# Kernel tuning notes

Measured on AMD Instinct MI355X. Metric: run time of the kernel, lower is better.

## Reference

```python
import jax, jax.numpy as jnp
import numpy as np

B = 32768          # batch rows
IN_DIM = 512
HID = 64           # hidden_dim fixed in module
COMM = 128         # output_dim == proto_latent_dim (num_simultaneous_tokens=1)
P = 2048           # num_protos
BETA = 0.25        # settings.alpha != 0
KL_W = 1.0         # settings.kl_weight
ENT_W = 0.1        # settings.entropy_weight
EPSILON = 1e-8


def setup_inputs() -> dict:
    key = jax.random.key(0)
    ks = jax.random.split(key, 16)
    s = 0.05
    return {
        "x": jax.random.normal(ks[0], (B, IN_DIM), jnp.float32),
        "eps": jax.random.normal(ks[1], (B, COMM), jnp.float32),
        "W_emb": jax.random.normal(ks[2], (IN_DIM, HID), jnp.float32) * s,
        "b_emb": jnp.zeros((HID,), jnp.float32),
        "W1": jax.random.normal(ks[3], (HID, HID), jnp.float32) * s,
        "b1": jnp.zeros((HID,), jnp.float32),
        "W2": jax.random.normal(ks[4], (HID, COMM), jnp.float32) * s,
        "b2": jnp.zeros((COMM,), jnp.float32),
        "W_mu": jax.random.normal(ks[5], (COMM, COMM), jnp.float32) * s,
        "b_mu": jnp.zeros((COMM,), jnp.float32),
        "W_var": jax.random.normal(ks[6], (COMM, COMM), jnp.float32) * s,
        "b_var": jnp.zeros((COMM,), jnp.float32),
        "protos": jax.random.uniform(ks[7], (P, COMM), jnp.float32, -1.0 / P, 1.0 / P),
    }


def _sq_dists(a, b):
    # ||a||^2 + ||b||^2 - 2 a b^T  -> [N, P] without [N,P,D] intermediate
    return (jnp.sum(a * a, axis=1, keepdims=True)
            + jnp.sum(b * b, axis=1)
            - 2.0 * a @ b.T)


def reference(x, eps, W_emb, b_emb, W1, b1, W2, b2, W_mu, b_mu, W_var, b_var, protos):
    sg = jax.lax.stop_gradient
    h = x @ W_emb + b_emb                       # [B, HID]
    h = h.reshape(-1, HID)                      # num_imgs = 1
    h = jax.nn.relu(h @ W1 + b1)
    h = jax.nn.relu(h @ W2 + b2)                # [B, COMM]
    r = h.reshape(-1, COMM)
    mu = r @ W_mu + b_mu
    logvar = r @ W_var + b_var
    sample = mu + jnp.exp(0.5 * logvar) * eps   # reparameterize

    # VQ: pairwise squared dists, argmin routing, codebook gather
    dists = _sq_dists(sample, protos)           # [B, P]
    idx = jnp.argmin(dists, axis=1)             # [B]
    quantized = protos[idx]                     # [B, COMM]

    commitment_loss = jnp.mean((sg(quantized) - mu) ** 2)
    embedding_loss = jnp.mean((quantized - sg(mu)) ** 2)
    vq_loss = BETA * commitment_loss + embedding_loss

    # entropy term: softmax-like row probs from Gaussian kernel on mu-proto dists
    # sum(((mu-p)/2)^2, -1) == ||mu-p||^2 / 4, computed via matmul form
    neg_dist = -0.5 * (_sq_dists(mu, protos) / 4.0)
    exponents = jnp.exp(neg_dist) + EPSILON     # [B, P]
    row_probs = exponents / jnp.sum(exponents, axis=1, keepdims=True)
    approx_probs = jnp.mean(row_probs, axis=0)  # [P]
    ent = jnp.sum(-approx_probs * jnp.log(approx_probs))
    vq_loss = vq_loss + ENT_W * ent

    # straight-through estimator
    q_st = sample + sg(quantized - sample)
    output = q_st.reshape(-1, COMM)

    kld = jnp.mean(-0.5 * jnp.sum(1.0 + logvar - mu ** 2 - jnp.exp(logvar), axis=1))
    total_loss = KL_W * kld + vq_loss
    return output, total_loss, kld
```

## Files before the change

### kernel.cpp

```cpp
#include <hip/hip_runtime.h>
#include <cmath>

constexpr int NB   = 32768;
constexpr int IND  = 512;
constexpr int HIDD = 64;
constexpr int CM   = 128;
constexpr int NP   = 2048;
constexpr float BETA  = 0.25f;
constexpr float ENT_W = 0.1f;
constexpr float EPSV  = 1e-8f;

typedef __attribute__((ext_vector_type(8))) short short8v;
typedef __attribute__((ext_vector_type(4))) float f32x4v;

__device__ __forceinline__ float4 ld4(const float* p){ return *reinterpret_cast<const float4*>(p); }
__device__ __forceinline__ void  st4(float* p, float4 v){ *reinterpret_cast<float4*>(p) = v; }

__device__ __forceinline__ unsigned short f2bf(float f){
  union { float f; unsigned u; } v; v.f = f;
  unsigned r = v.u + 0x7fffu + ((v.u >> 16) & 1u);
  return (unsigned short)(r >> 16);
}
__device__ __forceinline__ float bf2f(unsigned short u){
  union { unsigned u; float f; } v; v.u = ((unsigned)u) << 16;
  return v.f;
}
__device__ __forceinline__ short8v cvt8(float4 a, float4 b){
  short8v r;
  r[0]=(short)f2bf(a.x); r[1]=(short)f2bf(a.y); r[2]=(short)f2bf(a.z); r[3]=(short)f2bf(a.w);
  r[4]=(short)f2bf(b.x); r[5]=(short)f2bf(b.y); r[6]=(short)f2bf(b.z); r[7]=(short)f2bf(b.w);
  return r;
}

__device__ __forceinline__ float wave_sum(float v){
  #pragma unroll
  for (int m = 1; m < 64; m <<= 1) v += __shfl_xor(v, m, 64);
  return v;
}

typedef __attribute__((address_space(1))) unsigned int gu32;
typedef __attribute__((address_space(3))) unsigned int su32;
__device__ __forceinline__ void gload_lds16(const void* g, void* s){
  __builtin_amdgcn_global_load_lds((const gu32*)g, (su32*)s, 16, 0, 0);
}
__device__ __forceinline__ void gload_lds4(const void* g, void* s){
  __builtin_amdgcn_global_load_lds((const gu32*)g, (su32*)s, 4, 0, 0);
}
__device__ __forceinline__ void barrier_raw(){
  __builtin_amdgcn_sched_barrier(0);
  __builtin_amdgcn_s_barrier();
  __builtin_amdgcn_sched_barrier(0);
}

__global__ __launch_bounds__(256) void k_prep(const float* __restrict__ protos,
                                              float* __restrict__ normp2,
                                              unsigned short* __restrict__ pBF,
                                              const float* __restrict__ W_emb,
                                              const float* __restrict__ W1,
                                              const float* __restrict__ W2,
                                              const float* __restrict__ Wmu,
                                              const float* __restrict__ Wvar,
                                              unsigned short* __restrict__ WembT,
                                              unsigned short* __restrict__ W1T,
                                              unsigned short* __restrict__ W2T,
                                              unsigned short* __restrict__ WmuT,
                                              unsigned short* __restrict__ WvarT){
  const int b = blockIdx.x, tid = threadIdx.x;
  if (b < 8){
    const int p = b * 256 + tid;
    const float* row = protos + (size_t)p * CM;
    float s = 0.f;
    #pragma unroll
    for (int k = 0; k < CM; k += 4){
      float4 v = ld4(row + k);
      s += v.x*v.x + v.y*v.y + v.z*v.z + v.w*v.w;
      ushort4 u; u.x = f2bf(v.x); u.y = f2bf(v.y); u.z = f2bf(v.z); u.w = f2bf(v.w);
      *reinterpret_cast<ushort4*>(&pBF[(size_t)p * CM + k]) = u;
    }
    normp2[p] = s;
  } else if (b == 8){
    for (int i = tid; i < 512*64; i += 256){
      int k = i >> 6, n = i & 63;
      WembT[n*512 + k] = f2bf(W_emb[i]);
    }
  } else if (b == 9){
    for (int i = tid; i < 64*64; i += 256){
      int k = i >> 6, n = i & 63;
      W1T[n*64 + k] = f2bf(W1[i]);
    }
    for (int i = tid; i < 64*128; i += 256){
      int k = i >> 7, n = i & 127;
      W2T[n*64 + k] = f2bf(W2[i]);
    }
  } else if (b == 10){
    for (int i = tid; i < 128*128; i += 256){
      int k = i >> 7, n = i & 127;
      WmuT[n*128 + k] = f2bf(Wmu[i]);
    }
  } else {
    for (int i = tid; i < 128*128; i += 256){
      int k = i >> 7, n = i & 127;
      WvarT[n*128 + k] = f2bf(Wvar[i]);
    }
  }
}

__global__ __launch_bounds__(256, 2) void fwd_fused(const float* __restrict__ x,
    const unsigned short* __restrict__ WembT, const float* __restrict__ b_emb,
    const unsigned short* __restrict__ W1T,   const float* __restrict__ b1,
    const unsigned short* __restrict__ W2T,   const float* __restrict__ b2,
    const unsigned short* __restrict__ WmuT,  const float* __restrict__ bmu,
    const unsigned short* __restrict__ WvarT, const float* __restrict__ bvar,
    const float* __restrict__ epsIn,
    unsigned short* __restrict__ muBF, unsigned short* __restrict__ sBF,
    float* __restrict__ normMu2, float* __restrict__ kld_part){
  __shared__ __align__(16) unsigned short SH[16384];
  unsigned short* h1s = SH;
  unsigned short* h2s = SH + 4096;
  unsigned short* h3s = SH + 8192;
  unsigned short* muS = SH;
  unsigned short* sS  = SH + 8192;
  __shared__ float redbuf[4];

  const int tid = threadIdx.x;
  const int w = tid >> 6, l = tid & 63;
  const int lr = l >> 4, lc = l & 15;
  const int rowbase = blockIdx.x * 64;
  const int row = w*16 + lc;

  f32x4v acc1[4];
  #pragma unroll
  for (int nt = 0; nt < 4; nt++) acc1[nt] = (f32x4v){0.f,0.f,0.f,0.f};
  #pragma unroll 4
  for (int kc = 0; kc < IND; kc += 32){
    const float* xp = &x[(size_t)(rowbase + row) * IND + kc + lr*8];
    short8v af = cvt8(ld4(xp), ld4(xp + 4));
    #pragma unroll
    for (int nt = 0; nt < 4; nt++){
      const int n = nt*16 + lc;
      short8v bf = *reinterpret_cast<const short8v*>(&WembT[(size_t)n*512 + kc + lr*8]);
      acc1[nt] = __builtin_amdgcn_mfma_f32_16x16x32_bf16(af, bf, acc1[nt], 0, 0, 0);
    }
  }
  #pragma unroll
  for (int nt = 0; nt < 4; nt++){
    const int col = nt*16 + lc;
    const float bb = b_emb[col];
    #pragma unroll
    for (int r = 0; r < 4; r++){
      const int row2 = w*16 + lr*4 + r;
      h1s[(row2*64 + col) ^ ((row2 & 7) << 3)] = f2bf(acc1[nt][r] + bb);
    }
  }
  __syncthreads();

  f32x4v acc2[4];
  #pragma unroll
  for (int nt = 0; nt < 4; nt++) acc2[nt] = (f32x4v){0.f,0.f,0.f,0.f};
  #pragma unroll
  for (int ks = 0; ks < 2; ks++){
    const int ai = (row*64 + ks*32 + lr*8) ^ ((row & 7) << 3);
    short8v af = *reinterpret_cast<const short8v*>(&h1s[ai]);
    #pragma unroll
    for (int nt = 0; nt < 4; nt++){
      const int n = nt*16 + lc;
      short8v bf = *reinterpret_cast<const short8v*>(&W1T[(size_t)n*64 + ks*32 + lr*8]);
      acc2[nt] = __builtin_amdgcn_mfma_f32_16x16x32_bf16(af, bf, acc2[nt], 0, 0, 0);
    }
  }
  __syncthreads();
  #pragma unroll
  for (int nt = 0; nt < 4; nt++){
    const int col = nt*16 + lc;
    const float bb = b1[col];
    #pragma unroll
    for (int r = 0; r < 4; r++){
      const int row2 = w*16 + lr*4 + r;
      h2s[(row2*64 + col) ^ ((row2 & 7) << 3)] = f2bf(fmaxf(acc2[nt][r] + bb, 0.f));
    }
  }
  __syncthreads();

  f32x4v acc3[8];
  #pragma unroll
  for (int nt = 0; nt < 8; nt++) acc3[nt] = (f32x4v){0.f,0.f,0.f,0.f};
  #pragma unroll
  for (int ks = 0; ks < 2; ks++){
    const int ai = (row*64 + ks*32 + lr*8) ^ ((row & 7) << 3);
    short8v af = *reinterpret_cast<const short8v*>(&h2s[ai]);
    #pragma unroll
    for (int nt = 0; nt < 8; nt++){
      const int n = nt*16 + lc;
      short8v bf = *reinterpret_cast<const short8v*>(&W2T[(size_t)n*64 + ks*32 + lr*8]);
      acc3[nt] = __builtin_amdgcn_mfma_f32_16x16x32_bf16(af, bf, acc3[nt], 0, 0, 0);
    }
  }
  #pragma unroll
  for (int nt = 0; nt < 8; nt++){
    const int col = nt*16 + lc;
    const float bb = b2[col];
    #pragma unroll
    for (int r = 0; r < 4; r++){
      const int row2 = w*16 + lr*4 + r;
      h3s[(row2*128 + col) ^ ((row2 & 7) << 3)] = f2bf(fmaxf(acc3[nt][r] + bb, 0.f));
    }
  }
  __syncthreads();

  f32x4v accM[8], accV[8];
  #pragma unroll
  for (int nt = 0; nt < 8; nt++){ accM[nt] = (f32x4v){0.f,0.f,0.f,0.f}; accV[nt] = (f32x4v){0.f,0.f,0.f,0.f}; }
  #pragma unroll
  for (int ks = 0; ks < 4; ks++){
    const int ai = (row*128 + ks*32 + lr*8) ^ ((row & 7) << 3);
    short8v af = *reinterpret_cast<const short8v*>(&h3s[ai]);
    #pragma unroll
    for (int nt = 0; nt < 8; nt++){
      const int n = nt*16 + lc;
      short8v bM = *reinterpret_cast<const short8v*>(&WmuT [(size_t)n*128 + ks*32 + lr*8]);
      short8v bV = *reinterpret_cast<const short8v*>(&WvarT[(size_t)n*128 + ks*32 + lr*8]);
      accM[nt] = __builtin_amdgcn_mfma_f32_16x16x32_bf16(af, bM, accM[nt], 0, 0, 0);
      accV[nt] = __builtin_amdgcn_mfma_f32_16x16x32_bf16(af, bV, accV[nt], 0, 0, 0);
    }
  }
  __syncthreads();

  float kl = 0.f;
  float m2[4] = {0.f, 0.f, 0.f, 0.f};
  #pragma unroll
  for (int nt = 0; nt < 8; nt++){
    const int col = nt*16 + lc;
    const float bm = bmu[col], bv = bvar[col];
    #pragma unroll
    for (int r = 0; r < 4; r++){
      const int row2 = w*16 + lr*4 + r;
      const float mu = accM[nt][r] + bm;
      const float lv = accV[nt][r] + bv;
      const float s2 = __expf(0.5f * lv);
      const float sa = mu + s2 * epsIn[(size_t)(rowbase + row2)*CM + col];
      kl += 1.f + lv - mu*mu - s2*s2;
      m2[r] += mu*mu;
      const int li = (row2*128 + col) ^ ((row2 & 7) << 3);
      muS[li] = f2bf(mu);
      sS [li] = f2bf(sa);
    }
  }
  #pragma unroll
  for (int m = 1; m < 16; m <<= 1){
    #pragma unroll
    for (int r = 0; r < 4; r++) m2[r] += __shfl_xor(m2[r], m, 64);
  }
  if (lc == 0){
    #pragma unroll
    for (int r = 0; r < 4; r++) normMu2[rowbase + w*16 + lr*4 + r] = m2[r];
  }
  const float kw = wave_sum(kl);
  if (l == 0) redbuf[w] = kw;
  __syncthreads();
  if (tid == 0) kld_part[blockIdx.x] = redbuf[0]+redbuf[1]+redbuf[2]+redbuf[3];
  {
    const int r2 = tid >> 2, kq = tid & 3;
    #pragma unroll
    for (int i = 0; i < 4; i++){
      const int k = kq*32 + i*8;
      const int li = (r2*128 + k) ^ ((r2 & 7) << 3);
      short8v vm = *reinterpret_cast<const short8v*>(&muS[li]);
      short8v vs = *reinterpret_cast<const short8v*>(&sS[li]);
      *reinterpret_cast<short8v*>(&muBF[(size_t)(rowbase + r2)*CM + k]) = vm;
      *reinterpret_cast<short8v*>(&sBF [(size_t)(rowbase + r2)*CM + k]) = vs;
    }
  }
}

__global__ __launch_bounds__(512, 4) void proto_merged(
    const unsigned short* __restrict__ sBF, const unsigned short* __restrict__ mBF,
    const unsigned short* __restrict__ pBF, const float* __restrict__ normp2,
    const float* __restrict__ normMu2, const float* __restrict__ protosF,
    float* __restrict__ outA, float* __restrict__ approx_part,
    float* __restrict__ commit_part)
{
  __shared__ __align__(16) unsigned short Ps[3][64*CM];
  __shared__ float Pn[3][64];
  __shared__ float approxl[NP];
  __shared__ float bw[2][64];
  __shared__ int   iw[2][64];
  __shared__ float sw[2][64];
  __shared__ float srow_s[64];
  __shared__ int   bidx_s[64];
  __shared__ float redbuf[8];

  const int tid = threadIdx.x;
  const int w = tid >> 6, l = tid & 63;
  const int lr = l >> 4, lc = l & 15;
  const int rw = w & 1;
  const int pw = (w >> 1) & 1;
  const int mat = w >> 2;
  const int rowbase = blockIdx.x * 64;

  for (int t = tid; t < NP; t += 512) approxl[t] = 0.f;

  const unsigned short* Abase = mat ? mBF : sBF;
  short8v af[2][4];
  #pragma unroll
  for (int mt = 0; mt < 2; mt++){
    const size_t rg = (size_t)(rowbase + rw*32 + mt*16 + lc) * CM;
    #pragma unroll
    for (int ks = 0; ks < 4; ks++)
      af[mt][ks] = *reinterpret_cast<const short8v*>(&Abase[rg + ks*32 + lr*8]);
  }
  float nmn[8];
  #pragma unroll
  for (int mt = 0; mt < 2; mt++)
    #pragma unroll
    for (int r = 0; r < 4; r++)
      nmn[mt*4+r] = -0.125f * normMu2[rowbase + rw*32 + mt*16 + lr*4 + r];

  #define STAGE(pc, buf) {                                                        \
    _Pragma("unroll")                                                             \
    for (int j = 0; j < 2; j++){                                                  \
      const int p = w*8 + j*4 + (l >> 4);                                         \
      const int g = l & 15;                                                       \
      gload_lds16(&pBF[(size_t)((pc) + p)*CM + ((g*8) ^ ((p & 7)*8))],            \
                  &Ps[buf][(w*8 + j*4)*CM]);                                      \
    }                                                                             \
    if (w == 0) gload_lds4(&normp2[(pc) + l], &Pn[buf][0]);                       \
  }
  #define VWAIT_PEND() { if (w == 0) asm volatile("s_waitcnt vmcnt(3)" ::: "memory"); \
                         else        asm volatile("s_waitcnt vmcnt(2)" ::: "memory"); }
  #define VWAIT_ALL()  asm volatile("s_waitcnt vmcnt(0)" ::: "memory")

  float best[8]; int bidx[8]; float sr[8];
  #pragma unroll
  for (int i = 0; i < 8; i++){ best[i] = 3.4e38f; bidx[i] = 0; sr[i] = 0.f; }

  STAGE(0, 0);
  int cur = 0;
  for (int c = 0; c < 32; c++){
    const int nxt = (cur == 2) ? 0 : cur + 1;
    if (c < 31){ STAGE((c+1)*64, nxt); VWAIT_PEND(); }
    else       { VWAIT_ALL(); }
    barrier_raw();
    const float npv0 = Pn[cur][pw*32 + lc];
    const float npv1 = Pn[cur][pw*32 + 16 + lc];
    f32x4v acc[2][2];
    #pragma unroll
    for (int mt = 0; mt < 2; mt++)
      #pragma unroll
      for (int nt = 0; nt < 2; nt++) acc[mt][nt] = (f32x4v){0.f,0.f,0.f,0.f};
    #pragma unroll
    for (int ks = 0; ks < 4; ks++){
      const int pl0 = pw*32 + lc;
      const int pl1 = pw*32 + 16 + lc;
      short8v pf0 = *reinterpret_cast<const short8v*>(&Ps[cur][(pl0*CM + ks*32 + lr*8) ^ ((pl0 & 7) << 3)]);
      short8v pf1 = *reinterpret_cast<const short8v*>(&Ps[cur][(pl1*CM + ks*32 + lr*8) ^ ((pl1 & 7) << 3)]);
      #pragma unroll
      for (int mt = 0; mt < 2; mt++){
        acc[mt][0] = __builtin_amdgcn_mfma_f32_16x16x32_bf16(af[mt][ks], pf0, acc[mt][0], 0, 0, 0);
        acc[mt][1] = __builtin_amdgcn_mfma_f32_16x16x32_bf16(af[mt][ks], pf1, acc[mt][1], 0, 0, 0);
      }
    }
    const int pc = c*64;
    if (mat == 0){
      #pragma unroll
      for (int nt = 0; nt < 2; nt++){
        const int pg = pc + pw*32 + nt*16 + lc;
        const float npv = nt ? npv1 : npv0;
        #pragma unroll
        for (int mt = 0; mt < 2; mt++)
          #pragma unroll
          for (int r = 0; r < 4; r++){
            const float sc = fmaf(-2.f, acc[mt][nt][r], npv);
            if (sc < best[mt*4+r]){ best[mt*4+r] = sc; bidx[mt*4+r] = pg; }
          }
      }
    } else {
      #pragma unroll
      for (int nt = 0; nt < 2; nt++){
        const float pvn = -0.125f * (nt ? npv1 : npv0);
        #pragma unroll
        for (int mt = 0; mt < 2; mt++)
          #pragma unroll
          for (int r = 0; r < 4; r++)
            sr[mt*4+r] += __expf(fmaf(0.25f, acc[mt][nt][r], nmn[mt*4+r] + pvn));
      }
    }
    cur = nxt;
  }

  if (mat == 0){
    #pragma unroll
    for (int m = 1; m < 16; m <<= 1){
      #pragma unroll
      for (int i = 0; i < 8; i++){
        const float ob = __shfl_xor(best[i], m, 64);
        const int   oi = __shfl_xor(bidx[i], m, 64);
        if (ob < best[i] || (ob == best[i] && oi < bidx[i])){ best[i] = ob; bidx[i] = oi; }
      }
    }
    if (lc == 0){
      #pragma unroll
      for (int mt = 0; mt < 2; mt++)
        #pragma unroll
        for (int r = 0; r < 4; r++){
          const int row = rw*32 + mt*16 + lr*4 + r;
          bw[pw][row] = best[mt*4+r];
          iw[pw][row] = bidx[mt*4+r];
        }
    }
  } else {
    #pragma unroll
    for (int m = 1; m < 16; m <<= 1){
      #pragma unroll
      for (int i = 0; i < 8; i++) sr[i] += __shfl_xor(sr[i], m, 64);
    }
    if (lc == 0){
      #pragma unroll
      for (int mt = 0; mt < 2; mt++)
        #pragma unroll
        for (int r = 0; r < 4; r++){
          const int row = rw*32 + mt*16 + lr*4 + r;
          sw[pw][row] = sr[mt*4+r];
        }
    }
  }
  __syncthreads();
  if (tid < 64){
    float b0 = bw[0][tid]; int i0 = iw[0][tid];
    const float b1 = bw[1][tid]; const int i1 = iw[1][tid];
    if (b1 < b0 || (b1 == b0 && i1 < i0)){ b0 = b1; i0 = i1; }
    bidx_s[tid] = i0;
    srow_s[tid] = sw[0][tid] + sw[1][tid] + (float)NP * EPSV;
  }
  STAGE(0, 0);
  __syncthreads();

  {
    const int row = tid >> 3, cp = tid & 7;
    const int rowg = rowbase + row;
    const int idx = bidx_s[row];
    float cl = 0.f;
    #pragma unroll
    for (int c4 = 0; c4 < 4; c4++){
      const int cc = c4*32 + cp*4;
      float4 q = ld4(protosF + (size_t)idx * CM + cc);
      ushort4 mb = *reinterpret_cast<const ushort4*>(&mBF[(size_t)rowg * CM + cc]);
      st4(outA + (size_t)rowg * CM + cc, q);
      const float dx=q.x-bf2f(mb.x), dy=q.y-bf2f(mb.y), dz=q.z-bf2f(mb.z), dw=q.w-bf2f(mb.w);
      cl += dx*dx + dy*dy + dz*dz + dw*dw;
    }
    const float cw = wave_sum(cl);
    if (l == 0) redbuf[w] = cw;
  }
  float rs[8]; float epsc = 0.f;
  #pragma unroll
  for (int mt = 0; mt < 2; mt++)
    #pragma unroll
    for (int r = 0; r < 4; r++){
      rs[mt*4+r] = 1.0f / srow_s[rw*32 + mt*16 + lr*4 + r];
      epsc += rs[mt*4+r];
    }
  epsc *= EPSV;
  if (mat == 0){
    #pragma unroll
    for (int mt = 0; mt < 2; mt++){
      const size_t rg = (size_t)(rowbase + rw*32 + mt*16 + lc) * CM;
      #pragma unroll
      for (int ks = 0; ks < 4; ks++)
        af[mt][ks] = *reinterpret_cast<const short8v*>(&mBF[rg + ks*32 + lr*8]);
    }
  }
  __syncthreads();
  if (tid == 0) commit_part[blockIdx.x] = redbuf[0]+redbuf[1]+redbuf[2]+redbuf[3]
                                        + redbuf[4]+redbuf[5]+redbuf[6]+redbuf[7];

  const int pq = w >> 1;
  cur = 0;
  for (int c = 0; c < 32; c++){
    const int nxt = (cur == 2) ? 0 : cur + 1;
    if (c < 31){ STAGE((c+1)*64, nxt); VWAIT_PEND(); }
    else       { VWAIT_ALL(); }
    barrier_raw();
    const int pl = pq*16 + lc;
    const float npv = Pn[cur][pl];
    f32x4v accB[2];
    accB[0] = (f32x4v){0.f,0.f,0.f,0.f};
    accB[1] = (f32x4v){0.f,0.f,0.f,0.f};
    #pragma unroll
    for (int ks = 0; ks < 4; ks++){
      short8v pf = *reinterpret_cast<const short8v*>(&Ps[cur][(pl*CM + ks*32 + lr*8) ^ ((pl & 7) << 3)]);
      accB[0] = __builtin_amdgcn_mfma_f32_16x16x32_bf16(af[0][ks], pf, accB[0], 0, 0, 0);
      accB[1] = __builtin_amdgcn_mfma_f32_16x16x32_bf16(af[1][ks], pf, accB[1], 0, 0, 0);
    }
    const float pvn = -0.125f * npv;
    float cs = epsc;
    #pragma unroll
    for (int mt = 0; mt < 2; mt++)
      #pragma unroll
      for (int r = 0; r < 4; r++){
        const float e = __expf(fmaf(0.25f, accB[mt][r], nmn[mt*4+r] + pvn));
        cs = fmaf(e, rs[mt*4+r], cs);
      }
    cs += __shfl_xor(cs, 16, 64);
    cs += __shfl_xor(cs, 32, 64);
    if (l < 16) atomicAdd(&approxl[c*64 + pq*16 + lc], cs);
    cur = nxt;
  }
  __syncthreads();
  for (int t = tid; t < NP; t += 512)
    approx_part[(size_t)blockIdx.x * NP + t] = approxl[t];
  #undef STAGE
  #undef VWAIT_PEND
  #undef VWAIT_ALL
}

__global__ __launch_bounds__(256) void k4a(const float* __restrict__ approx_part,
                                           float* __restrict__ ent_part){
  __shared__ float red[128];
  const int tid = threadIdx.x;
  const int p = blockIdx.x * 32 + (tid & 31);
  const int slice = tid >> 5;
  float s = 0.f;
  for (int b = slice; b < 512; b += 8) s += approx_part[(size_t)b * NP + p];
  s += __shfl_xor(s, 32, 64);
  if ((tid & 63) < 32) red[(tid >> 6)*32 + (tid & 31)] = s;
  __syncthreads();
  if (tid < 32){
    const float a = (red[tid] + red[32+tid] + red[64+tid] + red[96+tid]) * (1.0f / 32768.0f);
    float t = -a * logf(a);
    #pragma unroll
    for (int m = 1; m < 32; m <<= 1) t += __shfl_xor(t, m, 32);
    if (tid == 0) ent_part[blockIdx.x] = t;
  }
}

__global__ __launch_bounds__(256) void k4b(const float* __restrict__ kld_part,
                                           const float* __restrict__ commit_part,
                                           const float* __restrict__ ent_part,
                                           float* __restrict__ outs){
  __shared__ float redbuf[8];
  const int tid = threadIdx.x;
  float k = 0.f, c = 0.f;
  for (int i = tid; i < 512; i += 256){ k += kld_part[i]; c += commit_part[i]; }
  float kw = wave_sum(k), cw = wave_sum(c);
  if ((tid & 63) == 0){ redbuf[tid >> 6] = kw; redbuf[4 + (tid >> 6)] = cw; }
  __syncthreads();
  if (tid == 0){
    float ks = redbuf[0] + redbuf[1] + redbuf[2] + redbuf[3];
    float cs = redbuf[4] + redbuf[5] + redbuf[6] + redbuf[7];
    float es = 0.f;
    for (int i = 0; i < 64; i++) es += ent_part[i];
    float kld = -0.5f * ks / 32768.0f;
    float m = cs / (32768.0f * 128.0f);
    float vq = BETA * m + m + ENT_W * es;
    outs[0] = kld + vq;
    outs[1] = kld;
  }
}

extern "C" void kernel_launch(void* const* d_in, const int* in_sizes, int n_in,
                              void* d_out, int out_size, void* d_ws, size_t ws_size,
                              hipStream_t stream){
  const float* x      = (const float*)d_in[0];
  const float* epsIn  = (const float*)d_in[1];
  const float* W_emb  = (const float*)d_in[2];
  const float* b_emb  = (const float*)d_in[3];
  const float* W1     = (const float*)d_in[4];
  const float* b1     = (const float*)d_in[5];
  const float* W2     = (const float*)d_in[6];
  const float* b2     = (const float*)d_in[7];
  const float* W_mu   = (const float*)d_in[8];
  const float* b_mu   = (const float*)d_in[9];
  const float* W_var  = (const float*)d_in[10];
  const float* b_var  = (const float*)d_in[11];
  const float* protos = (const float*)d_in[12];
  float* out = (float*)d_out;
  float* ws = (float*)d_ws;

  const size_t M1 = 1024u * 1024u;
  unsigned short* mBF  = (unsigned short*)ws;
  unsigned short* sBF  = (unsigned short*)(ws + 2*M1);
  float* approx_part = ws + 4*M1;
  float* tail = ws + 5*M1;
  float* normMu2     = tail;
  float* normp2      = normMu2 + 32768;
  float* kld_part    = normp2 + 2048;
  float* commit_part = kld_part + 512;
  float* ent_part    = commit_part + 512;
  unsigned short* pBF   = (unsigned short*)(ent_part + 64);
  unsigned short* WembT = pBF + (size_t)NP*CM;
  unsigned short* W1T   = WembT + 64*512;
  unsigned short* W2T   = W1T + 64*64;
  unsigned short* WmuT  = W2T + 128*64;
  unsigned short* WvarT = WmuT + 128*128;

  k_prep<<<12, 256, 0, stream>>>(protos, normp2, pBF, W_emb, W1, W2, W_mu, W_var,
                                 WembT, W1T, W2T, WmuT, WvarT);
  fwd_fused<<<NB/64, 256, 0, stream>>>(x, WembT, b_emb, W1T, b1, W2T, b2,
                                       WmuT, b_mu, WvarT, b_var, epsIn,
                                       mBF, sBF, normMu2, kld_part);
  proto_merged<<<NB/64, 512, 0, stream>>>(sBF, mBF, pBF, normp2, normMu2,
                                          protos, out, approx_part, commit_part);
  k4a<<<64, 256, 0, stream>>>(approx_part, ent_part);
  k4b<<<1, 256, 0, stream>>>(kld_part, commit_part, ent_part, out + (size_t)NB * CM);
}
```

Before: 190.2 us.

## Restructure proto pass: shared proto fragments for both mats, wider second pass

Each wave now computes both the sample-distance and mu-distance MFMAs against the same proto fragment, so one LDS read is reused across both matrices and the separate mat-split waves go away. The row-norm exponential is factored out of the per-element exp and folded into the row sum and weights. The second pass works on 128-proto chunks with double buffering and writes directly to global memory instead of going through LDS atomics. k_prep is spread over more blocks with coalesced writes, and fwd_fused's launch bounds allow more waves per SIMD. The cost is higher register pressure (two sets of A fragments plus 16 A fragments in pass two) and an extra barrier in every pass-two iteration.

```diff
diff --git a/kernel.cpp b/kernel.cpp
--- a/kernel.cpp
+++ b/kernel.cpp
@@ -78,34 +78,38 @@
       *reinterpret_cast<ushort4*>(&pBF[(size_t)p * CM + k]) = u;
     }
     normp2[p] = s;
-  } else if (b == 8){
-    for (int i = tid; i < 512*64; i += 256){
-      int k = i >> 6, n = i & 63;
-      WembT[n*512 + k] = f2bf(W_emb[i]);
-    }
-  } else if (b == 9){
+  } else if (b < 16){
+    const int nb = (b - 8) * 8;
+    for (int i = tid; i < 8*512; i += 256){
+      const int n = nb + (i >> 9), k = i & 511;
+      WembT[n*512 + k] = f2bf(W_emb[k*64 + n]);
+    }
+  } else if (b == 16){
     for (int i = tid; i < 64*64; i += 256){
-      int k = i >> 6, n = i & 63;
-      W1T[n*64 + k] = f2bf(W1[i]);
-    }
+      const int n = i >> 6, k = i & 63;
+      W1T[n*64 + k] = f2bf(W1[k*64 + n]);
+    }
+  } else if (b == 17){
+    for (int i = tid; i < 128*64; i += 256){
+      const int n = i >> 6, k = i & 63;
+      W2T[n*64 + k] = f2bf(W2[k*128 + n]);
+    }
+  } else if (b < 20){
+    const int nb = (b - 18) * 64;
     for (int i = tid; i < 64*128; i += 256){
-      int k = i >> 7, n = i & 127;
-      W2T[n*64 + k] = f2bf(W2[i]);
-    }
-  } else if (b == 10){
-    for (int i = tid; i < 128*128; i += 256){
-      int k = i >> 7, n = i & 127;
-      WmuT[n*128 + k] = f2bf(Wmu[i]);
+      const int n = nb + (i >> 7), k = i & 127;
+      WmuT[n*128 + k] = f2bf(Wmu[k*128 + n]);
     }
   } else {
-    for (int i = tid; i < 128*128; i += 256){
-      int k = i >> 7, n = i & 127;
-      WvarT[n*128 + k] = f2bf(Wvar[i]);
-    }
-  }
-}
-
-__global__ __launch_bounds__(256, 2) void fwd_fused(const float* __restrict__ x,
+    const int nb = (b - 20) * 64;
+    for (int i = tid; i < 64*128; i += 256){
+      const int n = nb + (i >> 7), k = i & 127;
+      WvarT[n*128 + k] = f2bf(Wvar[k*128 + n]);
+    }
+  }
+}
+
+__global__ __launch_bounds__(256, 4) void fwd_fused(const float* __restrict__ x,
     const unsigned short* __restrict__ WembT, const float* __restrict__ b_emb,
     const unsigned short* __restrict__ W1T,   const float* __restrict__ b1,
     const unsigned short* __restrict__ W2T,   const float* __restrict__ b2,
@@ -279,13 +283,14 @@
     float* __restrict__ outA, float* __restrict__ approx_part,
     float* __restrict__ commit_part)
 {
-  __shared__ __align__(16) unsigned short Ps[3][64*CM];
-  __shared__ float Pn[3][64];
-  __shared__ float approxl[NP];
-  __shared__ float bw[2][64];
-  __shared__ int   iw[2][64];
-  __shared__ float sw[2][64];
+  __shared__ __align__(16) unsigned short Ps[2][128*CM];
+  __shared__ float PnA[3][64];
+  __shared__ float PnB[2][128];
+  __shared__ float bw[4][64];
+  __shared__ int   iw[4][64];
+  __shared__ float sw[4][64];
   __shared__ float srow_s[64];
+  __shared__ float en_s[64];
   __shared__ int   bidx_s[64];
   __shared__ float redbuf[8];
 
@@ -293,145 +298,124 @@
   const int w = tid >> 6, l = tid & 63;
   const int lr = l >> 4, lc = l & 15;
   const int rw = w & 1;
-  const int pw = (w >> 1) & 1;
-  const int mat = w >> 2;
+  const int pq = w >> 1;
   const int rowbase = blockIdx.x * 64;
-
-  for (int t = tid; t < NP; t += 512) approxl[t] = 0.f;
-
-  const unsigned short* Abase = mat ? mBF : sBF;
-  short8v af[2][4];
+  unsigned short* PsFlat = &Ps[0][0];
+
+  short8v af_s[2][4], af_m[2][4];
   #pragma unroll
   for (int mt = 0; mt < 2; mt++){
     const size_t rg = (size_t)(rowbase + rw*32 + mt*16 + lc) * CM;
     #pragma unroll
-    for (int ks = 0; ks < 4; ks++)
-      af[mt][ks] = *reinterpret_cast<const short8v*>(&Abase[rg + ks*32 + lr*8]);
-  }
-  float nmn[8];
-  #pragma unroll
-  for (int mt = 0; mt < 2; mt++)
-    #pragma unroll
-    for (int r = 0; r < 4; r++)
-      nmn[mt*4+r] = -0.125f * normMu2[rowbase + rw*32 + mt*16 + lr*4 + r];
-
-  #define STAGE(pc, buf) {                                                        \
+    for (int ks = 0; ks < 4; ks++){
+      af_s[mt][ks] = *reinterpret_cast<const short8v*>(&sBF[rg + ks*32 + lr*8]);
+      af_m[mt][ks] = *reinterpret_cast<const short8v*>(&mBF[rg + ks*32 + lr*8]);
+    }
+  }
+
+  #define STAGE_A(pc, buf) {                                                      \
     _Pragma("unroll")                                                             \
     for (int j = 0; j < 2; j++){                                                  \
       const int p = w*8 + j*4 + (l >> 4);                                         \
       const int g = l & 15;                                                       \
       gload_lds16(&pBF[(size_t)((pc) + p)*CM + ((g*8) ^ ((p & 7)*8))],            \
-                  &Ps[buf][(w*8 + j*4)*CM]);                                      \
+                  PsFlat + (size_t)(buf)*8192 + (w*8 + j*4)*CM);                  \
     }                                                                             \
-    if (w == 0) gload_lds4(&normp2[(pc) + l], &Pn[buf][0]);                       \
-  }
-  #define VWAIT_PEND() { if (w == 0) asm volatile("s_waitcnt vmcnt(3)" ::: "memory"); \
-                         else        asm volatile("s_waitcnt vmcnt(2)" ::: "memory"); }
-  #define VWAIT_ALL()  asm volatile("s_waitcnt vmcnt(0)" ::: "memory")
+    if (w == 0) gload_lds4(&normp2[(pc) + l], &PnA[buf][0]);                      \
+  }
+  #define STAGE_B(pc, buf) {                                                      \
+    _Pragma("unroll")                                                             \
+    for (int j = 0; j < 4; j++){                                                  \
+      const int p = w*16 + j*4 + (l >> 4);                                        \
+      const int g = l & 15;                                                       \
+      gload_lds16(&pBF[(size_t)((pc) + p)*CM + ((g*8) ^ ((p & 7)*8))],            \
+                  &Ps[buf][(w*16 + j*4)*CM]);                                     \
+    }                                                                             \
+    if (w == 0){                                                                  \
+      gload_lds4(&normp2[(pc) + l],      &PnB[buf][0]);                           \
+      gload_lds4(&normp2[(pc) + 64 + l], &PnB[buf][64]);                          \
+    }                                                                             \
+  }
+  #define VWAIT_A()  { if (w == 0) asm volatile("s_waitcnt vmcnt(3)" ::: "memory"); \
+                       else        asm volatile("s_waitcnt vmcnt(2)" ::: "memory"); }
+  #define VWAIT_B()  { if (w == 0) asm volatile("s_waitcnt vmcnt(6)" ::: "memory"); \
+                       else        asm volatile("s_waitcnt vmcnt(4)" ::: "memory"); }
+  #define VWAIT_ALL() asm volatile("s_waitcnt vmcnt(0)" ::: "memory")
 
   float best[8]; int bidx[8]; float sr[8];
   #pragma unroll
   for (int i = 0; i < 8; i++){ best[i] = 3.4e38f; bidx[i] = 0; sr[i] = 0.f; }
 
-  STAGE(0, 0);
+  STAGE_A(0, 0);
   int cur = 0;
   for (int c = 0; c < 32; c++){
-    const int nxt = (cur == 2) ? 0 : cur + 1;
-    if (c < 31){ STAGE((c+1)*64, nxt); VWAIT_PEND(); }
+    const int nb = (cur == 2) ? 0 : cur + 1;
+    if (c < 31){ STAGE_A((c+1)*64, nb); VWAIT_A(); }
     else       { VWAIT_ALL(); }
     barrier_raw();
-    const float npv0 = Pn[cur][pw*32 + lc];
-    const float npv1 = Pn[cur][pw*32 + 16 + lc];
-    f32x4v acc[2][2];
+    const int pl = pq*16 + lc;
+    const float npv = PnA[cur][pl];
+    const float pvn = -0.125f * npv;
+    const unsigned short* pb = PsFlat + (size_t)cur*8192;
+    f32x4v as[2], am[2];
+    as[0] = (f32x4v){0.f,0.f,0.f,0.f}; as[1] = (f32x4v){0.f,0.f,0.f,0.f};
+    am[0] = (f32x4v){0.f,0.f,0.f,0.f}; am[1] = (f32x4v){0.f,0.f,0.f,0.f};
+    #pragma unroll
+    for (int ks = 0; ks < 4; ks++){
+      short8v pf = *reinterpret_cast<const short8v*>(&pb[(pl*CM + ks*32 + lr*8) ^ ((pl & 7) << 3)]);
+      as[0] = __builtin_amdgcn_mfma_f32_16x16x32_bf16(af_s[0][ks], pf, as[0], 0, 0, 0);
+      as[1] = __builtin_amdgcn_mfma_f32_16x16x32_bf16(af_s[1][ks], pf, as[1], 0, 0, 0);
+      am[0] = __builtin_amdgcn_mfma_f32_16x16x32_bf16(af_m[0][ks], pf, am[0], 0, 0, 0);
+      am[1] = __builtin_amdgcn_mfma_f32_16x16x32_bf16(af_m[1][ks], pf, am[1], 0, 0, 0);
+    }
+    const int pg = c*64 + pl;
     #pragma unroll
     for (int mt = 0; mt < 2; mt++)
       #pragma unroll
-      for (int nt = 0; nt < 2; nt++) acc[mt][nt] = (f32x4v){0.f,0.f,0.f,0.f};
-    #pragma unroll
-    for (int ks = 0; ks < 4; ks++){
-      const int pl0 = pw*32 + lc;
-      const int pl1 = pw*32 + 16 + lc;
-      short8v pf0 = *reinterpret_cast<const short8v*>(&Ps[cur][(pl0*CM + ks*32 + lr*8) ^ ((pl0 & 7) << 3)]);
-      short8v pf1 = *reinterpret_cast<const short8v*>(&Ps[cur][(pl1*CM + ks*32 + lr*8) ^ ((pl1 & 7) << 3)]);
+      for (int r = 0; r < 4; r++){
+        const float sc = fmaf(-2.f, as[mt][r], npv);
+        if (sc < best[mt*4+r]){ best[mt*4+r] = sc; bidx[mt*4+r] = pg; }
+        sr[mt*4+r] += __expf(fmaf(0.25f, am[mt][r], pvn));
+      }
+    cur = nb;
+  }
+
+  #pragma unroll
+  for (int m = 1; m < 16; m <<= 1){
+    #pragma unroll
+    for (int i = 0; i < 8; i++){
+      const float ob = __shfl_xor(best[i], m, 64);
+      const int   oi = __shfl_xor(bidx[i], m, 64);
+      if (ob < best[i] || (ob == best[i] && oi < bidx[i])){ best[i] = ob; bidx[i] = oi; }
+      sr[i] += __shfl_xor(sr[i], m, 64);
+    }
+  }
+  if (lc == 0){
+    #pragma unroll
+    for (int mt = 0; mt < 2; mt++)
       #pragma unroll
-      for (int mt = 0; mt < 2; mt++){
-        acc[mt][0] = __builtin_amdgcn_mfma_f32_16x16x32_bf16(af[mt][ks], pf0, acc[mt][0], 0, 0, 0);
-        acc[mt][1] = __builtin_amdgcn_mfma_f32_16x16x32_bf16(af[mt][ks], pf1, acc[mt][1], 0, 0, 0);
+      for (int r = 0; r < 4; r++){
+        const int row = rw*32 + mt*16 + lr*4 + r;
+        bw[pq][row] = best[mt*4+r];
+        iw[pq][row] = bidx[mt*4+r];
+        sw[pq][row] = sr[mt*4+r];
       }
-    }
-    const int pc = c*64;
-    if (mat == 0){
-      #pragma unroll
-      for (int nt = 0; nt < 2; nt++){
-        const int pg = pc + pw*32 + nt*16 + lc;
-        const float npv = nt ? npv1 : npv0;
-        #pragma unroll
-        for (int mt = 0; mt < 2; mt++)
-          #pragma unroll
-          for (int r = 0; r < 4; r++){
-            const float sc = fmaf(-2.f, acc[mt][nt][r], npv);
-            if (sc < best[mt*4+r]){ best[mt*4+r] = sc; bidx[mt*4+r] = pg; }
-          }
-      }
-    } else {
-      #pragma unroll
-      for (int nt = 0; nt < 2; nt++){
-        const float pvn = -0.125f * (nt ? npv1 : npv0);
-        #pragma unroll
-        for (int mt = 0; mt < 2; mt++)
-          #pragma unroll
-          for (int r = 0; r < 4; r++)
-            sr[mt*4+r] += __expf(fmaf(0.25f, acc[mt][nt][r], nmn[mt*4+r] + pvn));
-      }
-    }
-    cur = nxt;
-  }
-
-  if (mat == 0){
-    #pragma unroll
-    for (int m = 1; m < 16; m <<= 1){
-      #pragma unroll
-      for (int i = 0; i < 8; i++){
-        const float ob = __shfl_xor(best[i], m, 64);
-        const int   oi = __shfl_xor(bidx[i], m, 64);
-        if (ob < best[i] || (ob == best[i] && oi < bidx[i])){ best[i] = ob; bidx[i] = oi; }
-      }
-    }
-    if (lc == 0){
-      #pragma unroll
-      for (int mt = 0; mt < 2; mt++)
-        #pragma unroll
-        for (int r = 0; r < 4; r++){
-          const int row = rw*32 + mt*16 + lr*4 + r;
-          bw[pw][row] = best[mt*4+r];
-          iw[pw][row] = bidx[mt*4+r];
-        }
-    }
-  } else {
-    #pragma unroll
-    for (int m = 1; m < 16; m <<= 1){
-      #pragma unroll
-      for (int i = 0; i < 8; i++) sr[i] += __shfl_xor(sr[i], m, 64);
-    }
-    if (lc == 0){
-      #pragma unroll
-      for (int mt = 0; mt < 2; mt++)
-        #pragma unroll
-        for (int r = 0; r < 4; r++){
-          const int row = rw*32 + mt*16 + lr*4 + r;
-          sw[pw][row] = sr[mt*4+r];
-        }
-    }
-  }
-  __syncthreads();
+  }
+  __syncthreads();
+  STAGE_B(0, 0);
   if (tid < 64){
     float b0 = bw[0][tid]; int i0 = iw[0][tid];
-    const float b1 = bw[1][tid]; const int i1 = iw[1][tid];
-    if (b1 < b0 || (b1 == b0 && i1 < i0)){ b0 = b1; i0 = i1; }
+    #pragma unroll
+    for (int q = 1; q < 4; q++){
+      const float bq = bw[q][tid]; const int iq = iw[q][tid];
+      if (bq < b0 || (bq == b0 && iq < i0)){ b0 = bq; i0 = iq; }
+    }
     bidx_s[tid] = i0;
-    srow_s[tid] = sw[0][tid] + sw[1][tid] + (float)NP * EPSV;
-  }
-  STAGE(0, 0);
+    const float sraw = sw[0][tid] + sw[1][tid] + sw[2][tid] + sw[3][tid];
+    const float en = __expf(-0.125f * normMu2[rowbase + tid]);
+    en_s[tid] = en;
+    srow_s[tid] = fmaf(en, sraw, (float)NP * EPSV);
+  }
   __syncthreads();
 
   {
@@ -451,65 +435,64 @@
     const float cw = wave_sum(cl);
     if (l == 0) redbuf[w] = cw;
   }
-  float rs[8]; float epsc = 0.f;
-  #pragma unroll
-  for (int mt = 0; mt < 2; mt++)
+  float rs4[16]; float epsc = 0.f;
+  #pragma unroll
+  for (int mt = 0; mt < 4; mt++)
     #pragma unroll
     for (int r = 0; r < 4; r++){
-      rs[mt*4+r] = 1.0f / srow_s[rw*32 + mt*16 + lr*4 + r];
-      epsc += rs[mt*4+r];
+      const int row = mt*16 + lr*4 + r;
+      const float inv = 1.0f / srow_s[row];
+      rs4[mt*4+r] = en_s[row] * inv;
+      epsc += inv;
     }
   epsc *= EPSV;
-  if (mat == 0){
-    #pragma unroll
-    for (int mt = 0; mt < 2; mt++){
-      const size_t rg = (size_t)(rowbase + rw*32 + mt*16 + lc) * CM;
-      #pragma unroll
-      for (int ks = 0; ks < 4; ks++)
-        af[mt][ks] = *reinterpret_cast<const short8v*>(&mBF[rg + ks*32 + lr*8]);
-    }
+  short8v afB[4][4];
+  #pragma unroll
+  for (int mt = 0; mt < 4; mt++){
+    const size_t rg = (size_t)(rowbase + mt*16 + lc) * CM;
+    #pragma unroll
+    for (int ks = 0; ks < 4; ks++)
+      afB[mt][ks] = *reinterpret_cast<const short8v*>(&mBF[rg + ks*32 + lr*8]);
   }
   __syncthreads();
   if (tid == 0) commit_part[blockIdx.x] = redbuf[0]+redbuf[1]+redbuf[2]+redbuf[3]
                                         + redbuf[4]+redbuf[5]+redbuf[6]+redbuf[7];
 
-  const int pq = w >> 1;
-  cur = 0;
-  for (int c = 0; c < 32; c++){
-    const int nxt = (cur == 2) ? 0 : cur + 1;
-    if (c < 31){ STAGE((c+1)*64, nxt); VWAIT_PEND(); }
+  int curB = 0;
+  for (int c = 0; c < 16; c++){
+    if (c < 15){ STAGE_B((c+1)*128, curB ^ 1); VWAIT_B(); }
     else       { VWAIT_ALL(); }
     barrier_raw();
-    const int pl = pq*16 + lc;
-    const float npv = Pn[cur][pl];
-    f32x4v accB[2];
-    accB[0] = (f32x4v){0.f,0.f,0.f,0.f};
-    accB[1] = (f32x4v){0.f,0.f,0.f,0.f};
+    const int pl = w*16 + lc;
+    const float npv = PnB[curB][pl];
+    const float pvn = -0.125f * npv;
+    f32x4v acc[4];
+    #pragma unroll
+    for (int mt = 0; mt < 4; mt++) acc[mt] = (f32x4v){0.f,0.f,0.f,0.f};
     #pragma unroll
     for (int ks = 0; ks < 4; ks++){
-      short8v pf = *reinterpret_cast<const short8v*>(&Ps[cur][(pl*CM + ks*32 + lr*8) ^ ((pl & 7) << 3)]);
-      accB[0] = __builtin_amdgcn_mfma_f32_16x16x32_bf16(af[0][ks], pf, accB[0], 0, 0, 0);
-      accB[1] = __builtin_amdgcn_mfma_f32_16x16x32_bf16(af[1][ks], pf, accB[1], 0, 0, 0);
-    }
-    const float pvn = -0.125f * npv;
+      short8v pf = *reinterpret_cast<const short8v*>(&Ps[curB][(pl*CM + ks*32 + lr*8) ^ ((pl & 7) << 3)]);
+      acc[0] = __builtin_amdgcn_mfma_f32_16x16x32_bf16(afB[0][ks], pf, acc[0], 0, 0, 0);
+      acc[1] = __builtin_amdgcn_mfma_f32_16x16x32_bf16(afB[1][ks], pf, acc[1], 0, 0, 0);
+      acc[2] = __builtin_amdgcn_mfma_f32_16x16x32_bf16(afB[2][ks], pf, acc[2], 0, 0, 0);
+      acc[3] = __builtin_amdgcn_mfma_f32_16x16x32_bf16(afB[3][ks], pf, acc[3], 0, 0, 0);
+    }
     float cs = epsc;
     #pragma unroll
-    for (int mt = 0; mt < 2; mt++)
+    for (int mt = 0; mt < 4; mt++)
       #pragma unroll
-      for (int r = 0; r < 4; r++){
-        const float e = __expf(fmaf(0.25f, accB[mt][r], nmn[mt*4+r] + pvn));
-        cs = fmaf(e, rs[mt*4+r], cs);
-      }
+      for (int r = 0; r < 4; r++)
+        cs = fmaf(__expf(fmaf(0.25f, acc[mt][r], pvn)), rs4[mt*4+r], cs);
     cs += __shfl_xor(cs, 16, 64);
     cs += __shfl_xor(cs, 32, 64);
-    if (l < 16) atomicAdd(&approxl[c*64 + pq*16 + lc], cs);
-    cur = nxt;
-  }
-  __syncthreads();
-  for (int t = tid; t < NP; t += 512)
-    approx_part[(size_t)blockIdx.x * NP + t] = approxl[t];
-  #undef STAGE
-  #undef VWAIT_PEND
+    if (l < 16) approx_part[(size_t)blockIdx.x * NP + c*128 + pl] = cs;
+    barrier_raw();
+    curB ^= 1;
+  }
+  #undef STAGE_A
+  #undef STAGE_B
+  #undef VWAIT_A
+  #undef VWAIT_B
   #undef VWAIT_ALL
 }
 
@@ -593,7 +576,7 @@
   unsigned short* WmuT  = W2T + 128*64;
   unsigned short* WvarT = WmuT + 128*128;
 
-  k_prep<<<12, 256, 0, stream>>>(protos, normp2, pBF, W_emb, W1, W2, W_mu, W_var,
+  k_prep<<<22, 256, 0, stream>>>(protos, normp2, pBF, W_emb, W1, W2, W_mu, W_var,
                                  WembT, W1T, W2T, WmuT, WvarT);
   fwd_fused<<<NB/64, 256, 0, stream>>>(x, WembT, b_emb, W1T, b1, W2T, b2,
                                        WmuT, b_mu, WvarT, b_var, epsIn,
```

Result: faster. 185.9 us (-2.3%).

## Stage x tile through swizzled LDS, split weight prep across more blocks, raise occupancy

Applied to the files above, without the earlier changes.

The first GEMM in fwd_fused now loads each 64-column chunk of x with coalesced float4 reads by all threads, converts it to bf16 into a swizzled LDS tile, and feeds the MFMAs from LDS. Previously each lane did strided row loads directly from global memory. The weight transpose/convert prep is spread over 22 blocks instead of 12, with write-coalesced indexing. Launch bounds are raised to 4 waves-per-EU blocks to increase occupancy. The costs are two __syncthreads per chunk, extra LDS use, and possible register pressure from the tighter launch bound.

```diff
diff --git a/kernel.cpp b/kernel.cpp
--- a/kernel.cpp
+++ b/kernel.cpp
@@ -78,34 +78,38 @@
       *reinterpret_cast<ushort4*>(&pBF[(size_t)p * CM + k]) = u;
     }
     normp2[p] = s;
-  } else if (b == 8){
-    for (int i = tid; i < 512*64; i += 256){
-      int k = i >> 6, n = i & 63;
-      WembT[n*512 + k] = f2bf(W_emb[i]);
-    }
-  } else if (b == 9){
+  } else if (b < 16){
+    const int nb = (b - 8) * 8;
+    for (int i = tid; i < 8*512; i += 256){
+      const int n = nb + (i >> 9), k = i & 511;
+      WembT[n*512 + k] = f2bf(W_emb[k*64 + n]);
+    }
+  } else if (b == 16){
     for (int i = tid; i < 64*64; i += 256){
-      int k = i >> 6, n = i & 63;
-      W1T[n*64 + k] = f2bf(W1[i]);
-    }
+      const int n = i >> 6, k = i & 63;
+      W1T[n*64 + k] = f2bf(W1[k*64 + n]);
+    }
+  } else if (b == 17){
+    for (int i = tid; i < 128*64; i += 256){
+      const int n = i >> 6, k = i & 63;
+      W2T[n*64 + k] = f2bf(W2[k*128 + n]);
+    }
+  } else if (b < 20){
+    const int nb = (b - 18) * 64;
     for (int i = tid; i < 64*128; i += 256){
-      int k = i >> 7, n = i & 127;
-      W2T[n*64 + k] = f2bf(W2[i]);
-    }
-  } else if (b == 10){
-    for (int i = tid; i < 128*128; i += 256){
-      int k = i >> 7, n = i & 127;
-      WmuT[n*128 + k] = f2bf(Wmu[i]);
+      const int n = nb + (i >> 7), k = i & 127;
+      WmuT[n*128 + k] = f2bf(Wmu[k*128 + n]);
     }
   } else {
-    for (int i = tid; i < 128*128; i += 256){
-      int k = i >> 7, n = i & 127;
-      WvarT[n*128 + k] = f2bf(Wvar[i]);
-    }
-  }
-}
-
-__global__ __launch_bounds__(256, 2) void fwd_fused(const float* __restrict__ x,
+    const int nb = (b - 20) * 64;
+    for (int i = tid; i < 64*128; i += 256){
+      const int n = nb + (i >> 7), k = i & 127;
+      WvarT[n*128 + k] = f2bf(Wvar[k*128 + n]);
+    }
+  }
+}
+
+__global__ __launch_bounds__(256, 4) void fwd_fused(const float* __restrict__ x,
     const unsigned short* __restrict__ WembT, const float* __restrict__ b_emb,
     const unsigned short* __restrict__ W1T,   const float* __restrict__ b1,
     const unsigned short* __restrict__ W2T,   const float* __restrict__ b2,
@@ -115,6 +119,7 @@
     unsigned short* __restrict__ muBF, unsigned short* __restrict__ sBF,
     float* __restrict__ normMu2, float* __restrict__ kld_part){
   __shared__ __align__(16) unsigned short SH[16384];
+  __shared__ __align__(16) unsigned short Xs[4096];
   unsigned short* h1s = SH;
   unsigned short* h2s = SH + 4096;
   unsigned short* h3s = SH + 8192;
@@ -131,15 +136,29 @@
   f32x4v acc1[4];
   #pragma unroll
   for (int nt = 0; nt < 4; nt++) acc1[nt] = (f32x4v){0.f,0.f,0.f,0.f};
-  #pragma unroll 4
-  for (int kc = 0; kc < IND; kc += 32){
-    const float* xp = &x[(size_t)(rowbase + row) * IND + kc + lr*8];
-    short8v af = cvt8(ld4(xp), ld4(xp + 4));
-    #pragma unroll
-    for (int nt = 0; nt < 4; nt++){
-      const int n = nt*16 + lc;
-      short8v bf = *reinterpret_cast<const short8v*>(&WembT[(size_t)n*512 + kc + lr*8]);
-      acc1[nt] = __builtin_amdgcn_mfma_f32_16x16x32_bf16(af, bf, acc1[nt], 0, 0, 0);
+  const int srow = tid >> 2, sq = tid & 3;
+  const float* xrow = x + (size_t)(rowbase + srow) * IND + sq*16;
+  for (int kc8 = 0; kc8 < 8; kc8++){
+    float4 v0 = ld4(xrow + kc8*64);
+    float4 v1 = ld4(xrow + kc8*64 + 4);
+    float4 v2 = ld4(xrow + kc8*64 + 8);
+    float4 v3 = ld4(xrow + kc8*64 + 12);
+    __syncthreads();
+    const int b0 = (srow*64 + sq*16)     ^ ((srow & 7) << 3);
+    const int b1i = (srow*64 + sq*16 + 8) ^ ((srow & 7) << 3);
+    *reinterpret_cast<short8v*>(&Xs[b0])  = cvt8(v0, v1);
+    *reinterpret_cast<short8v*>(&Xs[b1i]) = cvt8(v2, v3);
+    __syncthreads();
+    #pragma unroll
+    for (int ks = 0; ks < 2; ks++){
+      const int ai = (row*64 + ks*32 + lr*8) ^ ((row & 7) << 3);
+      short8v af = *reinterpret_cast<const short8v*>(&Xs[ai]);
+      #pragma unroll
+      for (int nt = 0; nt < 4; nt++){
+        const int n = nt*16 + lc;
+        short8v bf = *reinterpret_cast<const short8v*>(&WembT[(size_t)n*512 + kc8*64 + ks*32 + lr*8]);
+        acc1[nt] = __builtin_amdgcn_mfma_f32_16x16x32_bf16(af, bf, acc1[nt], 0, 0, 0);
+      }
     }
   }
   #pragma unroll
@@ -593,7 +612,7 @@
   unsigned short* WmuT  = W2T + 128*64;
   unsigned short* WvarT = WmuT + 128*128;
 
-  k_prep<<<12, 256, 0, stream>>>(protos, normp2, pBF, W_emb, W1, W2, W_mu, W_var,
+  k_prep<<<22, 256, 0, stream>>>(protos, normp2, pBF, W_emb, W1, W2, W_mu, W_var,
                                  WembT, W1T, W2T, WmuT, WvarT);
   fwd_fused<<<NB/64, 256, 0, stream>>>(x, WembT, b_emb, W1T, b1, W2T, b2,
                                        WmuT, b_mu, WvarT, b_var, epsIn,
```

Result: faster. 165.7 us (-12.9%).
